# Optimization experiments

Hardware: AMD Instinct MI355X
Metric: run time of the kernel (lower is better)

The kernel has to match this reference:

```python
import jax, jax.numpy as jnp
import numpy as np

B, N, NH, F = 4, 4096, 16, 8      # batch, grid cells, input points per cell, raw features
D, FF, H, PE = 256, 1024, 8, 32   # model_dim, ff_dim, n_heads, pos_emb_dim
NG, NI = 8192, 65536              # grid table size, input-point table size
SEQ = 4                           # 4 ** seq_level
HD = D // H


def layer_norm(x, g, b, eps=1e-5):
    mu = jnp.mean(x, axis=-1, keepdims=True)
    var = jnp.mean(jnp.square(x - mu), axis=-1, keepdims=True)
    return (x - mu) * jax.lax.rsqrt(var + eps) * g + b


def setup_inputs() -> dict:
    key = jax.random.key(0)
    ks = jax.random.split(key, 20)
    inp = {}
    inp["x"] = jax.random.normal(ks[0], (B, N, NH, F), jnp.float32)
    inp["grid_level_indices"] = jax.random.randint(ks[1], (B, N), 0, NG)
    inp["drop_mask"] = jax.random.bernoulli(ks[2], 0.1, (B, N))
    # buffers
    inp["input_mapping"] = jax.random.randint(ks[3], (NG, NH), 0, NI)
    inp["in_range"] = jax.random.bernoulli(ks[4], 0.95, (NG, NH))
    inp["input_coordinates"] = jax.random.uniform(ks[5], (2, NI), jnp.float32, -3.14, 3.14)
    inp["grid_coords"] = jax.random.uniform(ks[6], (2, NG), jnp.float32, -3.14, 3.14)
    # params
    inp["W_in"] = jax.random.normal(ks[7], (F, D), jnp.float32) * 0.05
    inp["b_in"] = jnp.zeros((D,), jnp.float32)
    inp["W_pe"] = jax.random.normal(ks[8], (2, PE), jnp.float32) * 0.2
    inp["W_bias"] = jax.random.normal(ks[9], (PE, H), jnp.float32) * 0.1
    inp["W_v"] = jax.random.normal(ks[10], (D, D), jnp.float32) * 0.02
    inp["W_o"] = jax.random.normal(ks[11], (D, D), jnp.float32) * 0.02
    inp["W1"] = jax.random.normal(ks[12], (D, FF), jnp.float32) * 0.02
    inp["W2"] = jax.random.normal(ks[13], (FF, D), jnp.float32) * 0.02
    inp["g1"] = jnp.ones((D,), jnp.float32)
    inp["b1"] = jnp.zeros((D,), jnp.float32)
    inp["g2"] = jnp.ones((D,), jnp.float32)
    inp["b2"] = jnp.zeros((D,), jnp.float32)
    return inp


def reference(x, grid_level_indices, drop_mask, input_mapping, in_range,
              input_coordinates, grid_coords, W_in, b_in, W_pe, W_bias,
              W_v, W_o, W1, W2, g1, b1, g2, b2):
    b, n, nh, _ = x.shape
    nq = n // SEQ
    K = SEQ * nh  # keys per group

    # input_layer.input_mlp: Linear + SiLU
    x = jax.nn.silu(x @ W_in + b_in)                       # [b,n,nh,D]

    # relative positions (polar): grid-cell coords vs gathered input-point coords
    gseq = grid_level_indices.reshape(b, nq, SEQ)
    idx = input_mapping[gseq]                              # [b,nq,4,nh]
    lon1 = grid_coords[0][gseq][..., None, None]           # [b,nq,4,1,1]
    lat1 = grid_coords[1][gseq][..., None, None]
    lon2 = input_coordinates[0][idx][:, :, None]           # [b,nq,1,4,nh]
    lat2 = input_coordinates[1][idx][:, :, None]
    dlon, dlat = lon2 - lon1, lat2 - lat1                  # [b,nq,4,4,nh]
    dist = jnp.sqrt(dlon * dlon + dlat * dlat + 1e-12)
    ang = jnp.arctan2(dlat, dlon)
    pos1 = dist.reshape(b, nq, SEQ, K)
    pos2 = ang.reshape(b, nq, SEQ, K)

    # mask: out-of-range OR dropped, broadcast across the 4 query cells
    m = (~in_range[grid_level_indices]) | drop_mask[:, :, None]  # [b,n,nh]
    m = m.reshape(b, nq, SEQ, nh)
    mask = jnp.broadcast_to(m[:, :, None], (b, nq, SEQ, SEQ, nh)).reshape(b, nq, SEQ, K)

    xs = x.reshape(b, nq, K, D)                            # kv tokens per group

    # positional bias -> attention scores (qkv_bias=False path: bias-only scores)
    pe = jax.nn.silu(jnp.stack([pos1, pos2], -1) @ W_pe)   # [b,nq,4,K,PE]
    bias = pe @ W_bias                                     # [b,nq,4,K,H]
    scores = jnp.moveaxis(bias, -1, 2)                     # [b,nq,H,4,K]
    scores = jnp.where(mask[:, :, None], -1e9, scores)
    att = jax.nn.softmax(scores, axis=-1)

    vh = (xs @ W_v).reshape(b, nq, K, H, HD)
    out = jnp.einsum('bqhtk,bqkhd->bqthd', att, vh).reshape(b, nq, SEQ, D)
    out = out @ W_o                                        # [b,nq,4,D]

    # nha_layer tail (q_res=False, dropout=0)
    h = layer_norm(out, g1, b1)
    h = layer_norm(h + jax.nn.silu(h @ W1) @ W2, g2, b2)
    return h.reshape(b, n, D)
```

## Files before the change

### kernel.cpp

```cpp
#include <hip/hip_runtime.h>

#define B_   4
#define N_   4096
#define NH_  16
#define F_   8
#define D_   256
#define FF_  1024
#define H_   8
#define PE_  32
#define NG_  8192
#define NI_  65536
#define NQ_  1024

typedef short short8 __attribute__((ext_vector_type(8)));
typedef short short4v __attribute__((ext_vector_type(4)));
typedef float f32x4 __attribute__((ext_vector_type(4)));

__device__ __forceinline__ float silu_f(float v) {
  return v * __builtin_amdgcn_rcpf(1.f + __expf(-v));
}
__device__ __forceinline__ unsigned short f2bf(float f) {
  unsigned int x = __float_as_uint(f);
  unsigned int r = (x + 0x7fffu + ((x >> 16) & 1u)) >> 16;
  return (unsigned short)r;
}
__device__ __forceinline__ float bf2f(unsigned short h) {
  return __uint_as_float(((unsigned int)h) << 16);
}

__device__ __forceinline__ int detect_layout(const unsigned int* w) {
  unsigned b1 = 0, b0 = 0;
#pragma unroll
  for (int i = 0; i < 64; ++i) {
    unsigned v = w[i];
    b1 |= v & 0x0000FF00u;
    b0 |= v & 0x000000FFu;
  }
  return b1 ? 0 : (b0 ? 1 : 2);
}
__device__ __forceinline__ int read_bool(const void* p, int i, int lay) {
  if (lay == 0) return ((const unsigned char*)p)[i] != 0;
  if (lay == 1) return ((const int*)p)[i] != 0;
  return ((const float*)p)[i] != 0.0f;
}

#define WOP_OFF 0
#define W1P_OFF 65536
#define W2P_OFF (65536 + 262144)
#define WVP_OFF (65536 + 262144 + 262144)
#define WIP_OFF (65536 + 262144 + 262144 + 65536)
#define WBP_OFF (WIP_OFF + 8192)
#define WS_TAIL ((65536 + 262144 + 262144) * 2)
#define WS_FULL ((WBP_OFF + 512) * 2)

__global__ __launch_bounds__(256) void k_pack(
    const float* __restrict__ Wo, const float* __restrict__ W1,
    const float* __restrict__ W2, const float* __restrict__ Wv,
    const float* __restrict__ Wi, const float* __restrict__ Wb,
    short* __restrict__ ws)
{
  int t = blockIdx.x * 256 + threadIdx.x;
  if (t < 8192) {
    int g = t & 3, n = (t >> 2) & 255, kk = t >> 10;
    int k0 = kk * 32 + g * 8;
    short8 v;
#pragma unroll
    for (int j = 0; j < 8; ++j) v[j] = (short)f2bf(Wo[(k0 + j) * 256 + n]);
    *(short8*)(ws + WOP_OFF + t * 8) = v;
  } else if (t < 40960) {
    int u = t - 8192;
    int g = u & 3, n = (u >> 2) & 1023, kk = u >> 12;
    int k0 = kk * 32 + g * 8;
    short8 v;
#pragma unroll
    for (int j = 0; j < 8; ++j) v[j] = (short)f2bf(W1[(k0 + j) * 1024 + n]);
    *(short8*)(ws + W1P_OFF + u * 8) = v;
  } else if (t < 73728) {
    int u = t - 40960;
    int g = u & 3, n = (u >> 2) & 255, kk = u >> 10;
    int k0 = kk * 32 + g * 8;
    short8 v;
#pragma unroll
    for (int j = 0; j < 8; ++j) v[j] = (short)f2bf(W2[(k0 + j) * 256 + n]);
    *(short8*)(ws + W2P_OFF + u * 8) = v;
  } else if (t < 81920) {
    int u = t - 73728;
    int g = u & 3, n = (u >> 2) & 255, kk = u >> 10;
    int k0 = kk * 32 + g * 8;
    short8 v;
#pragma unroll
    for (int j = 0; j < 8; ++j) v[j] = (short)f2bf(Wv[(k0 + j) * 256 + n]);
    *(short8*)(ws + WVP_OFF + u * 8) = v;
  } else if (t < 82944) {
    int u = t - 81920;
    int g = u & 3, n = u >> 2;
    short8 v;
#pragma unroll
    for (int j = 0; j < 8; ++j) {
      int k = g * 8 + j;
      v[j] = (k < 8) ? (short)f2bf(Wi[k * 256 + n]) : (short)0;
    }
    *(short8*)(ws + WIP_OFF + (n * 4 + g) * 8) = v;
  } else if (t < 83008) {
    int u = t - 82944;
    int g = u & 3, col = u >> 2;
    short8 v;
#pragma unroll
    for (int j = 0; j < 8; ++j) {
      int p = g * 8 + j;
      v[j] = (col < 8) ? (short)f2bf(Wb[p * 8 + col]) : (short)0;
    }
    *(short8*)(ws + WBP_OFF + (col * 4 + g) * 8) = v;
  }
}

#define OFF_XST   0
#define OFF_ATTB  32768
#define OFF_XL    36864
#define OFF_DIST  36864
#define OFF_ANG   37888
#define OFF_KLON  38912
#define OFF_KLAT  39168
#define OFF_KMSK  39424
#define OFF_GLON  39680
#define OFF_GLAT  39696
#define OFF_GIDX  39712
#define OFF_DROP  39728

__global__ __launch_bounds__(256) void k_attn_mfma(
    const float* __restrict__ x, const int* __restrict__ gli,
    const void* __restrict__ drop, const int* __restrict__ imap,
    const void* __restrict__ inr, const float* __restrict__ icoord,
    const float* __restrict__ gcoord, const float* __restrict__ W_pe,
    const float* __restrict__ b_in, const short* __restrict__ WiP,
    const short* __restrict__ WbP, const short* __restrict__ WvP,
    float* __restrict__ out)
{
  __shared__ __align__(16) char sm[39744];
  float* xl = (float*)(sm + OFF_XL);
  float* distl = (float*)(sm + OFF_DIST);
  float* angl = (float*)(sm + OFF_ANG);
  float* klon = (float*)(sm + OFF_KLON);
  float* klat = (float*)(sm + OFF_KLAT);
  int* kmask = (int*)(sm + OFF_KMSK);
  float* glon = (float*)(sm + OFF_GLON);
  float* glat = (float*)(sm + OFF_GLAT);
  int* gidx = (int*)(sm + OFF_GIDX);
  int* dropf = (int*)(sm + OFF_DROP);

  const int grp = blockIdx.x;
  const int b = grp >> 10;
  const int q = grp & (NQ_ - 1);
  const int tid = threadIdx.x;
  const int w = tid >> 6;
  const int l15 = tid & 15;
  const int g = (tid & 63) >> 4;
  const int swz = (l15 & 7) << 4;

  const int lay = detect_layout((const unsigned int*)inr);

  if (tid < 4) {
    int gg = gli[b * N_ + q * 4 + tid];
    gidx[tid] = gg;
    glon[tid] = gcoord[gg];
    glat[tid] = gcoord[NG_ + gg];
    dropf[tid] = read_bool(drop, b * N_ + q * 4 + tid, lay);
  }
  const float* xb = x + (size_t)(b * N_ + q * 4) * (NH_ * F_);
  xl[tid] = xb[tid];
  xl[tid + 256] = xb[tid + 256];
  __syncthreads();

  if (tid < 64) {
    int s = tid >> 4;
    int gg = gidx[s];
    int id = imap[gg * NH_ + (tid & 15)];
    klon[tid] = icoord[id];
    klat[tid] = icoord[NI_ + id];
    kmask[tid] = (read_bool(inr, gg * NH_ + (tid & 15), lay) == 0) | dropf[s];
  }

  {
    short8 a = {0, 0, 0, 0, 0, 0, 0, 0};
    if (g == 0) {
      const float4* xlf = (const float4*)xl;
      float4 xa = xlf[(w * 16 + l15) * 2];
      float4 xc = xlf[(w * 16 + l15) * 2 + 1];
      a[0] = (short)f2bf(xa.x); a[1] = (short)f2bf(xa.y);
      a[2] = (short)f2bf(xa.z); a[3] = (short)f2bf(xa.w);
      a[4] = (short)f2bf(xc.x); a[5] = (short)f2bf(xc.y);
      a[6] = (short)f2bf(xc.z); a[7] = (short)f2bf(xc.w);
    }
    const int k0 = w * 16 + g * 4;
#pragma unroll
    for (int nf = 0; nf < 16; ++nf) {
      short8 bv = *(const short8*)(WiP + ((nf * 16 + l15) * 4 + g) * 8);
      f32x4 accM = {0.f, 0.f, 0.f, 0.f};
      accM = __builtin_amdgcn_mfma_f32_16x16x32_bf16(a, bv, accM, 0, 0, 0);
      int d = nf * 16 + l15;
      float bn = b_in[d];
      short4v pv;
#pragma unroll
      for (int r = 0; r < 4; ++r)
        pv[r] = (short)f2bf(silu_f(accM[r] + bn));
      *(short4v*)(sm + ((d * 128 + k0 * 2) ^ ((d & 7) << 4))) = pv;
    }
  }
  __syncthreads();

  {
    const int t = tid >> 6, k = tid & 63;
    float dlon = klon[k] - glon[t];
    float dlat = klat[k] - glat[t];
    distl[tid] = sqrtf(dlon * dlon + dlat * dlat + 1e-12f);
    angl[tid] = atan2f(dlat, dlon);
  }
  __syncthreads();

  {
    float wpe0[8], wpe1[8];
    {
      const float4* wp = (const float4*)W_pe;
      float4 w0a = wp[g * 2], w0b = wp[g * 2 + 1];
      float4 w1a = wp[8 + g * 2], w1b = wp[8 + g * 2 + 1];
      wpe0[0] = w0a.x; wpe0[1] = w0a.y; wpe0[2] = w0a.z; wpe0[3] = w0a.w;
      wpe0[4] = w0b.x; wpe0[5] = w0b.y; wpe0[6] = w0b.z; wpe0[7] = w0b.w;
      wpe1[0] = w1a.x; wpe1[1] = w1a.y; wpe1[2] = w1a.z; wpe1[3] = w1a.w;
      wpe1[4] = w1b.x; wpe1[5] = w1b.y; wpe1[6] = w1b.z; wpe1[7] = w1b.w;
    }
    short8 wb = *(const short8*)(WbP + (l15 * 4 + g) * 8);
    f32x4 accS[4];
#pragma unroll
    for (int i = 0; i < 4; ++i) {
      int row = (w * 4 + i) * 16 + l15;
      float dd = distl[row];
      float aa = angl[row];
      short8 pa;
#pragma unroll
      for (int j = 0; j < 8; ++j)
        pa[j] = (short)f2bf(silu_f(fmaf(dd, wpe0[j], aa * wpe1[j])));
      f32x4 z = {0.f, 0.f, 0.f, 0.f};
      accS[i] = __builtin_amdgcn_mfma_f32_16x16x32_bf16(pa, wb, z, 0, 0, 0);
    }
    float sv[16];
    float mx = -1e30f;
#pragma unroll
    for (int i = 0; i < 4; ++i)
#pragma unroll
      for (int r = 0; r < 4; ++r) {
        int k = i * 16 + g * 4 + r;
        float s = kmask[k] ? -1e9f : accS[i][r];
        sv[i * 4 + r] = s;
        mx = fmaxf(mx, s);
      }
    mx = fmaxf(mx, __shfl_xor(mx, 16));
    mx = fmaxf(mx, __shfl_xor(mx, 32));
    float sum = 0.f;
#pragma unroll
    for (int u = 0; u < 16; ++u) { sv[u] = __expf(sv[u] - mx); sum += sv[u]; }
    sum += __shfl_xor(sum, 16);
    sum += __shfl_xor(sum, 32);
    float inv = __builtin_amdgcn_rcpf(sum);
    if (l15 < 8) {
      int row = l15 * 4 + w;
      int rs = (row & 7) << 4;
#pragma unroll
      for (int i = 0; i < 4; ++i) {
        short4v pv;
#pragma unroll
        for (int r = 0; r < 4; ++r) pv[r] = (short)f2bf(sv[i * 4 + r] * inv);
        *(short4v*)(sm + OFF_ATTB + ((row * 128 + (i * 16 + g * 4) * 2) ^ rs)) = pv;
      }
    }
  }
  __syncthreads();

  f32x4 accY[2][4];
  {
    f32x4 z = {0.f, 0.f, 0.f, 0.f};
#pragma unroll
    for (int mi = 0; mi < 2; ++mi)
#pragma unroll
      for (int ni = 0; ni < 4; ++ni) accY[mi][ni] = z;
  }
#pragma unroll
  for (int kk = 0; kk < 2; ++kk) {
    short8 a0 = *(const short8*)(sm + OFF_ATTB + ((l15 * 128 + kk * 64 + g * 16) ^ swz));
    short8 a1 = *(const short8*)(sm + OFF_ATTB + (((16 + l15) * 128 + kk * 64 + g * 16) ^ swz));
    short8 bf[4];
#pragma unroll
    for (int ni = 0; ni < 4; ++ni)
      bf[ni] = *(const short8*)(sm +
          (((w * 64 + ni * 16 + l15) * 128 + kk * 64 + g * 16) ^ swz));
#pragma unroll
    for (int ni = 0; ni < 4; ++ni) {
      accY[0][ni] = __builtin_amdgcn_mfma_f32_16x16x32_bf16(a0, bf[ni], accY[0][ni], 0, 0, 0);
      accY[1][ni] = __builtin_amdgcn_mfma_f32_16x16x32_bf16(a1, bf[ni], accY[1][ni], 0, 0, 0);
    }
  }
  __syncthreads();

#pragma unroll
  for (int mi = 0; mi < 2; ++mi)
#pragma unroll
    for (int ni = 0; ni < 4; ++ni)
#pragma unroll
      for (int r = 0; r < 4; ++r) {
        int row = mi * 16 + g * 4 + r;
        int col = w * 64 + ni * 16 + l15;
        *(unsigned short*)(sm + ((row * 512 + col * 2) ^ ((row & 7) << 4))) =
            f2bf(accY[mi][ni][r]);
      }
  __syncthreads();

  {
    const int mf = w >> 1;
    f32x4 accV[4];
    {
      f32x4 z = {0.f, 0.f, 0.f, 0.f};
#pragma unroll
      for (int ni = 0; ni < 4; ++ni) accV[ni] = z;
    }
#pragma unroll
    for (int kk = 0; kk < 8; ++kk) {
      short8 a = *(const short8*)(sm +
          (((mf * 16 + l15) * 512 + kk * 64 + g * 16) ^ swz));
#pragma unroll
      for (int ni = 0; ni < 4; ++ni) {
        int col = w * 64 + ni * 16 + l15;
        short8 bv = *(const short8*)(WvP + ((size_t)(kk * 256 + col)) * 32 + g * 8);
        accV[ni] = __builtin_amdgcn_mfma_f32_16x16x32_bf16(a, bv, accV[ni], 0, 0, 0);
      }
    }
    float* outl = (float*)(sm + 16384);
    const int gb = (w & 1) * 2;
#pragma unroll
    for (int ni = 0; ni < 4; ++ni) {
      if (g == gb + (ni >> 1)) {
#pragma unroll
        for (int r = 0; r < 4; ++r)
          outl[r * 256 + w * 64 + ni * 16 + l15] = accV[ni][r];
      }
    }
  }
  __syncthreads();

  {
    const float* outl = (const float*)(sm + 16384);
    float* ob = out + (size_t)grp * (4 * D_);
#pragma unroll
    for (int t = 0; t < 4; ++t) ob[t * 256 + tid] = outl[t * 256 + tid];
  }
}

__global__ __launch_bounds__(256) void k_attn_valu(
    const float* __restrict__ x, const int* __restrict__ gli,
    const void* __restrict__ drop, const int* __restrict__ imap,
    const void* __restrict__ inr, const float* __restrict__ icoord,
    const float* __restrict__ gcoord, const float* __restrict__ W_in,
    const float* __restrict__ b_in, const float* __restrict__ W_pe,
    const float* __restrict__ W_bias, const float* __restrict__ W_v,
    float* __restrict__ out)
{
  __shared__ __align__(16) float xl[512];
  __shared__ float glon[4], glat[4];
  __shared__ int gidx[4], dropf[4];
  __shared__ float klon[64], klat[64];
  __shared__ int kmask[64];
  __shared__ __align__(16) unsigned short xs[64 * D_];
  __shared__ __align__(16) float att[32 * 64];
  __shared__ __align__(16) float yl[4 * 8 * 260];

  const int grp = blockIdx.x;
  const int b = grp >> 10;
  const int q = grp & (NQ_ - 1);
  const int tid = threadIdx.x;
  const int lay = detect_layout((const unsigned int*)inr);

  if (tid < 4) {
    int g = gli[b * N_ + q * 4 + tid];
    gidx[tid] = g;
    glon[tid] = gcoord[g];
    glat[tid] = gcoord[NG_ + g];
    dropf[tid] = read_bool(drop, b * N_ + q * 4 + tid, lay);
  }
  const float* xb = x + (size_t)(b * N_ + q * 4) * (NH_ * F_);
  xl[tid] = xb[tid];
  xl[tid + 256] = xb[tid + 256];
  __syncthreads();

  if (tid < 64) {
    int s = tid >> 4;
    int g = gidx[s];
    int id = imap[g * NH_ + (tid & 15)];
    klon[tid] = icoord[id];
    klat[tid] = icoord[NI_ + id];
    kmask[tid] = (read_bool(inr, g * NH_ + (tid & 15), lay) == 0) | dropf[s];
  }
  {
    float w[8];
#pragma unroll
    for (int c = 0; c < 8; ++c) w[c] = W_in[c * D_ + tid];
    float bi = b_in[tid];
#pragma unroll 4
    for (int k = 0; k < 64; ++k) {
      float v = bi;
#pragma unroll
      for (int c = 0; c < 8; ++c) v = fmaf(xl[k * 8 + c], w[c], v);
      xs[k * D_ + tid] = f2bf(silu_f(v));
    }
  }
  __syncthreads();
  {
    const int t = tid >> 6, k = tid & 63;
    float dlon = klon[k] - glon[t];
    float dlat = klat[k] - glat[t];
    float dist = sqrtf(dlon * dlon + dlat * dlat + 1e-12f);
    float ang = atan2f(dlat, dlon);
    float bias[8];
#pragma unroll
    for (int h = 0; h < 8; ++h) bias[h] = 0.f;
#pragma unroll
    for (int p = 0; p < 32; ++p) {
      float pv = silu_f(fmaf(dist, W_pe[p], ang * W_pe[32 + p]));
#pragma unroll
      for (int h = 0; h < 8; ++h) bias[h] = fmaf(pv, W_bias[p * 8 + h], bias[h]);
    }
    const bool mk = (kmask[k] != 0);
#pragma unroll
    for (int h = 0; h < 8; ++h)
      att[(h * 4 + t) * 64 + k] = mk ? -1e9f : bias[h];
  }
  __syncthreads();
  {
    const int row = tid >> 3, l8 = tid & 7;
    float sv[8];
    float mx = -1e30f;
#pragma unroll
    for (int i = 0; i < 8; ++i) { sv[i] = att[row * 64 + l8 + i * 8]; mx = fmaxf(mx, sv[i]); }
#pragma unroll
    for (int off = 1; off < 8; off <<= 1) mx = fmaxf(mx, __shfl_xor(mx, off, 8));
    float sm = 0.f;
#pragma unroll
    for (int i = 0; i < 8; ++i) { sv[i] = __expf(sv[i] - mx); sm += sv[i]; }
#pragma unroll
    for (int off = 1; off < 8; off <<= 1) sm += __shfl_xor(sm, off, 8);
    float inv = 1.f / sm;
#pragma unroll
    for (int i = 0; i < 8; ++i) att[row * 64 + l8 + i * 8] = sv[i] * inv;
  }
  __syncthreads();
  {
    float acc[32];
#pragma unroll
    for (int r = 0; r < 32; ++r) acc[r] = 0.f;
    for (int k4 = 0; k4 < 64; k4 += 4) {
      float xv0 = bf2f(xs[(k4 + 0) * D_ + tid]);
      float xv1 = bf2f(xs[(k4 + 1) * D_ + tid]);
      float xv2 = bf2f(xs[(k4 + 2) * D_ + tid]);
      float xv3 = bf2f(xs[(k4 + 3) * D_ + tid]);
#pragma unroll
      for (int r = 0; r < 32; ++r) {
        float4 a = *(const float4*)&att[r * 64 + k4];
        acc[r] = fmaf(a.x, xv0, acc[r]);
        acc[r] = fmaf(a.y, xv1, acc[r]);
        acc[r] = fmaf(a.z, xv2, acc[r]);
        acc[r] = fmaf(a.w, xv3, acc[r]);
      }
    }
#pragma unroll
    for (int r = 0; r < 32; ++r)
      yl[(r & 3) * 2080 + (r >> 2) * 260 + tid] = acc[r];
  }
  __syncthreads();
  {
    const int h = tid >> 5;
    float o0 = 0.f, o1 = 0.f, o2 = 0.f, o3 = 0.f;
    for (int c = 0; c < 256; c += 4) {
      float w0 = W_v[(c + 0) * D_ + tid];
      float w1 = W_v[(c + 1) * D_ + tid];
      float w2 = W_v[(c + 2) * D_ + tid];
      float w3 = W_v[(c + 3) * D_ + tid];
      float4 y0 = *(const float4*)&yl[0 * 2080 + h * 260 + c];
      float4 y1 = *(const float4*)&yl[1 * 2080 + h * 260 + c];
      float4 y2 = *(const float4*)&yl[2 * 2080 + h * 260 + c];
      float4 y3 = *(const float4*)&yl[3 * 2080 + h * 260 + c];
      o0 = fmaf(y0.x, w0, o0); o0 = fmaf(y0.y, w1, o0); o0 = fmaf(y0.z, w2, o0); o0 = fmaf(y0.w, w3, o0);
      o1 = fmaf(y1.x, w0, o1); o1 = fmaf(y1.y, w1, o1); o1 = fmaf(y1.z, w2, o1); o1 = fmaf(y1.w, w3, o1);
      o2 = fmaf(y2.x, w0, o2); o2 = fmaf(y2.y, w1, o2); o2 = fmaf(y2.z, w2, o2); o2 = fmaf(y2.w, w3, o2);
      o3 = fmaf(y3.x, w0, o3); o3 = fmaf(y3.y, w1, o3); o3 = fmaf(y3.z, w2, o3); o3 = fmaf(y3.w, w3, o3);
    }
    float* ob = out + (size_t)grp * (4 * D_);
    ob[0 * D_ + tid] = o0;
    ob[1 * D_ + tid] = o1;
    ob[2 * D_ + tid] = o2;
    ob[3 * D_ + tid] = o3;
  }
}

__device__ __forceinline__ void gemm_acc8(
    f32x4 acc[4][4], const unsigned short* As, const short* Bp,
    int N, int kk0, int colbase, int l15, int g)
{
#pragma unroll
  for (int kk = 0; kk < 8; ++kk) {
    short8 a[4], bv[4];
#pragma unroll
    for (int mi = 0; mi < 4; ++mi) {
      int row = mi * 16 + l15;
      int byte = (row * 512 + kk * 64 + g * 16) ^ ((row & 7) << 4);
      a[mi] = *(const short8*)((const char*)As + byte);
    }
#pragma unroll
    for (int ni = 0; ni < 4; ++ni) {
      int col = colbase + ni * 16 + l15;
      size_t off = ((size_t)(kk0 + kk) * N + col) * 32 + g * 8;
      bv[ni] = *(const short8*)(Bp + off);
    }
#pragma unroll
    for (int mi = 0; mi < 4; ++mi)
#pragma unroll
      for (int ni = 0; ni < 4; ++ni)
        acc[mi][ni] = __builtin_amdgcn_mfma_f32_16x16x32_bf16(
            a[mi], bv[ni], acc[mi][ni], 0, 0, 0);
  }
}

__global__ __launch_bounds__(256) void k_tail_mfma(
    const float* __restrict__ g1v, const float* __restrict__ b1v,
    const float* __restrict__ g2v, const float* __restrict__ b2v,
    const short* __restrict__ WoP, const short* __restrict__ W1P,
    const short* __restrict__ W2P, float* __restrict__ io)
{
  __shared__ __align__(16) unsigned short sA1[64 * 256];
  __shared__ __align__(16) unsigned short sU[64 * 256];
  __shared__ float sPs[4][64];
  __shared__ float sPss[4][64];

  const int tid = threadIdx.x;
  const int w = tid >> 6;
  const int l = tid & 63;
  const int l15 = l & 15;
  const int g = l >> 4;
  float* base = io + (size_t)blockIdx.x * (64 * 256);

#pragma unroll
  for (int i = 0; i < 16; ++i) {
    int e = (tid + 256 * i) * 4;
    int row = e >> 8, c = e & 255;
    float4 v = *(const float4*)(base + e);
    unsigned int lo = (unsigned int)f2bf(v.x) | ((unsigned int)f2bf(v.y) << 16);
    unsigned int hi = (unsigned int)f2bf(v.z) | ((unsigned int)f2bf(v.w) << 16);
    int byte = (row * 512 + c * 2) ^ ((row & 7) << 4);
    *(uint2*)((char*)sU + byte) = make_uint2(lo, hi);
  }
  __syncthreads();

  f32x4 acc[4][4];
  {
    f32x4 z = {0.f, 0.f, 0.f, 0.f};
#pragma unroll
    for (int mi = 0; mi < 4; ++mi)
#pragma unroll
      for (int ni = 0; ni < 4; ++ni) acc[mi][ni] = z;
  }
  gemm_acc8(acc, sU, WoP, 256, 0, w * 64, l15, g);

#pragma unroll
  for (int mi = 0; mi < 4; ++mi)
#pragma unroll
    for (int r = 0; r < 4; ++r) {
      float a0 = acc[mi][0][r], a1 = acc[mi][1][r], a2 = acc[mi][2][r], a3 = acc[mi][3][r];
      float s = a0 + a1 + a2 + a3;
      float ss = a0 * a0 + a1 * a1 + a2 * a2 + a3 * a3;
#pragma unroll
      for (int off = 1; off < 16; off <<= 1) {
        s += __shfl_xor(s, off);
        ss += __shfl_xor(ss, off);
      }
      if (l15 == 0) {
        int row = 16 * mi + 4 * g + r;
        sPs[w][row] = s;
        sPss[w][row] = ss;
      }
    }
  __syncthreads();

  {
    float ga[4], bb[4];
#pragma unroll
    for (int ni = 0; ni < 4; ++ni) {
      int col = 64 * w + 16 * ni + l15;
      ga[ni] = g1v[col];
      bb[ni] = b1v[col];
    }
#pragma unroll
    for (int mi = 0; mi < 4; ++mi)
#pragma unroll
      for (int r = 0; r < 4; ++r) {
        int row = 16 * mi + 4 * g + r;
        float S = sPs[0][row] + sPs[1][row] + sPs[2][row] + sPs[3][row];
        float SS = sPss[0][row] + sPss[1][row] + sPss[2][row] + sPss[3][row];
        float mu = S * (1.f / 256.f);
        float rs = rsqrtf(SS * (1.f / 256.f) - mu * mu + 1e-5f);
#pragma unroll
        for (int ni = 0; ni < 4; ++ni) {
          int col = 64 * w + 16 * ni + l15;
          float val = (acc[mi][ni][r] - mu) * rs * ga[ni] + bb[ni];
          acc[mi][ni][r] = val;
          int byte = (row * 512 + col * 2) ^ ((row & 7) << 4);
          *(unsigned short*)((char*)sA1 + byte) = f2bf(val);
        }
      }
  }
  __syncthreads();

  for (int p = 0; p < 4; ++p) {
    f32x4 acc2[4][4];
    {
      f32x4 z = {0.f, 0.f, 0.f, 0.f};
#pragma unroll
      for (int mi = 0; mi < 4; ++mi)
#pragma unroll
        for (int ni = 0; ni < 4; ++ni) acc2[mi][ni] = z;
    }
    gemm_acc8(acc2, sA1, W1P, 1024, 0, p * 256 + w * 64, l15, g);
#pragma unroll
    for (int mi = 0; mi < 4; ++mi)
#pragma unroll
      for (int ni = 0; ni < 4; ++ni)
#pragma unroll
        for (int r = 0; r < 4; ++r) {
          int row = 16 * mi + 4 * g + r;
          int col = 64 * w + 16 * ni + l15;
          int byte = (row * 512 + col * 2) ^ ((row & 7) << 4);
          *(unsigned short*)((char*)sU + byte) = f2bf(silu_f(acc2[mi][ni][r]));
        }
    __syncthreads();
    gemm_acc8(acc, sU, W2P, 256, p * 8, w * 64, l15, g);
    __syncthreads();
  }

#pragma unroll
  for (int mi = 0; mi < 4; ++mi)
#pragma unroll
    for (int r = 0; r < 4; ++r) {
      float a0 = acc[mi][0][r], a1 = acc[mi][1][r], a2 = acc[mi][2][r], a3 = acc[mi][3][r];
      float s = a0 + a1 + a2 + a3;
      float ss = a0 * a0 + a1 * a1 + a2 * a2 + a3 * a3;
#pragma unroll
      for (int off = 1; off < 16; off <<= 1) {
        s += __shfl_xor(s, off);
        ss += __shfl_xor(ss, off);
      }
      if (l15 == 0) {
        int row = 16 * mi + 4 * g + r;
        sPs[w][row] = s;
        sPss[w][row] = ss;
      }
    }
  __syncthreads();

  {
    float ga[4], bb[4];
#pragma unroll
    for (int ni = 0; ni < 4; ++ni) {
      int col = 64 * w + 16 * ni + l15;
      ga[ni] = g2v[col];
      bb[ni] = b2v[col];
    }
#pragma unroll
    for (int mi = 0; mi < 4; ++mi)
#pragma unroll
      for (int r = 0; r < 4; ++r) {
        int row = 16 * mi + 4 * g + r;
        float S = sPs[0][row] + sPs[1][row] + sPs[2][row] + sPs[3][row];
        float SS = sPss[0][row] + sPss[1][row] + sPss[2][row] + sPss[3][row];
        float mu = S * (1.f / 256.f);
        float rs = rsqrtf(SS * (1.f / 256.f) - mu * mu + 1e-5f);
#pragma unroll
        for (int ni = 0; ni < 4; ++ni) {
          int col = 64 * w + 16 * ni + l15;
          base[row * 256 + col] = (acc[mi][ni][r] - mu) * rs * ga[ni] + bb[ni];
        }
      }
  }
}

__global__ __launch_bounds__(256) void k_tail(
    const float* __restrict__ Wo, const float* __restrict__ W1,
    const float* __restrict__ W2, const float* __restrict__ g1,
    const float* __restrict__ b1, const float* __restrict__ g2,
    const float* __restrict__ b2, float* __restrict__ io)
{
  __shared__ __align__(16) float rl[16 * 260];
  __shared__ __align__(16) float h1[16 * 260];
  __shared__ __align__(16) unsigned short u[16 * FF_];
  const int tid = threadIdx.x;
  float* base = io + (size_t)blockIdx.x * (16 * D_);

#pragma unroll
  for (int r = 0; r < 16; ++r) rl[r * 260 + tid] = base[r * D_ + tid];
  __syncthreads();
  {
    float acc[16];
#pragma unroll
    for (int r = 0; r < 16; ++r) acc[r] = 0.f;
    for (int c = 0; c < 256; c += 4) {
      float w0 = Wo[(c + 0) * D_ + tid], w1 = Wo[(c + 1) * D_ + tid];
      float w2 = Wo[(c + 2) * D_ + tid], w3 = Wo[(c + 3) * D_ + tid];
#pragma unroll
      for (int r = 0; r < 16; ++r) {
        float4 rv = *(const float4*)&rl[r * 260 + c];
        acc[r] = fmaf(rv.x, w0, acc[r]); acc[r] = fmaf(rv.y, w1, acc[r]);
        acc[r] = fmaf(rv.z, w2, acc[r]); acc[r] = fmaf(rv.w, w3, acc[r]);
      }
    }
#pragma unroll
    for (int r = 0; r < 16; ++r) h1[r * 260 + tid] = acc[r];
  }
  __syncthreads();
  {
    const int r = tid >> 4, l = tid & 15;
    float s = 0.f, ss = 0.f;
#pragma unroll
    for (int i = 0; i < 16; ++i) { float v = h1[r * 260 + l + i * 16]; s += v; ss += v * v; }
#pragma unroll
    for (int off = 1; off < 16; off <<= 1) { s += __shfl_xor(s, off, 16); ss += __shfl_xor(ss, off, 16); }
    float mu = s * (1.f / 256.f);
    float rs = rsqrtf(ss * (1.f / 256.f) - mu * mu + 1e-5f);
#pragma unroll
    for (int i = 0; i < 16; ++i) {
      int d = l + i * 16;
      h1[r * 260 + d] = (h1[r * 260 + d] - mu) * rs * g1[d] + b1[d];
    }
  }
  __syncthreads();
  for (int fo = 0; fo < 4; ++fo) {
    const int f = fo * 256 + tid;
    float a2[16];
#pragma unroll
    for (int r = 0; r < 16; ++r) a2[r] = 0.f;
    for (int c = 0; c < 256; c += 4) {
      float w0 = W1[(c + 0) * FF_ + f], w1 = W1[(c + 1) * FF_ + f];
      float w2 = W1[(c + 2) * FF_ + f], w3 = W1[(c + 3) * FF_ + f];
#pragma unroll
      for (int r = 0; r < 16; ++r) {
        float4 hv = *(const float4*)&h1[r * 260 + c];
        a2[r] = fmaf(hv.x, w0, a2[r]); a2[r] = fmaf(hv.y, w1, a2[r]);
        a2[r] = fmaf(hv.z, w2, a2[r]); a2[r] = fmaf(hv.w, w3, a2[r]);
      }
    }
#pragma unroll
    for (int r = 0; r < 16; ++r) u[r * FF_ + f] = f2bf(silu_f(a2[r]));
  }
  __syncthreads();
  {
    float a3[16];
#pragma unroll
    for (int r = 0; r < 16; ++r) a3[r] = h1[r * 260 + tid];
    for (int f = 0; f < FF_; f += 8) {
      float w[8];
#pragma unroll
      for (int i = 0; i < 8; ++i) w[i] = W2[(f + i) * D_ + tid];
#pragma unroll
      for (int r = 0; r < 16; ++r) {
        uint4 uv = *(const uint4*)&u[r * FF_ + f];
        a3[r] = fmaf(__uint_as_float(uv.x << 16), w[0], a3[r]);
        a3[r] = fmaf(__uint_as_float(uv.x & 0xffff0000u), w[1], a3[r]);
        a3[r] = fmaf(__uint_as_float(uv.y << 16), w[2], a3[r]);
        a3[r] = fmaf(__uint_as_float(uv.y & 0xffff0000u), w[3], a3[r]);
        a3[r] = fmaf(__uint_as_float(uv.z << 16), w[4], a3[r]);
        a3[r] = fmaf(__uint_as_float(uv.z & 0xffff0000u), w[5], a3[r]);
        a3[r] = fmaf(__uint_as_float(uv.w << 16), w[6], a3[r]);
        a3[r] = fmaf(__uint_as_float(uv.w & 0xffff0000u), w[7], a3[r]);
      }
    }
#pragma unroll
    for (int r = 0; r < 16; ++r) rl[r * 260 + tid] = a3[r];
  }
  __syncthreads();
  {
    const int r = tid >> 4, l = tid & 15;
    float s = 0.f, ss = 0.f;
#pragma unroll
    for (int i = 0; i < 16; ++i) { float v = rl[r * 260 + l + i * 16]; s += v; ss += v * v; }
#pragma unroll
    for (int off = 1; off < 16; off <<= 1) { s += __shfl_xor(s, off, 16); ss += __shfl_xor(ss, off, 16); }
    float mu = s * (1.f / 256.f);
    float rs = rsqrtf(ss * (1.f / 256.f) - mu * mu + 1e-5f);
#pragma unroll
    for (int i = 0; i < 16; ++i) {
      int d = l + i * 16;
      base[r * D_ + d] = (rl[r * 260 + d] - mu) * rs * g2[d] + b2[d];
    }
  }
}

extern "C" void kernel_launch(void* const* d_in, const int* in_sizes, int n_in,
                              void* d_out, int out_size, void* d_ws, size_t ws_size,
                              hipStream_t stream) {
  (void)in_sizes; (void)n_in; (void)out_size;
  const float* x = (const float*)d_in[0];
  const int* gli = (const int*)d_in[1];
  const void* drop = d_in[2];
  const int* imap = (const int*)d_in[3];
  const void* inr = d_in[4];
  const float* icoord = (const float*)d_in[5];
  const float* gcoord = (const float*)d_in[6];
  const float* W_in = (const float*)d_in[7];
  const float* b_in = (const float*)d_in[8];
  const float* W_pe = (const float*)d_in[9];
  const float* W_bias = (const float*)d_in[10];
  const float* W_v = (const float*)d_in[11];
  const float* W_o = (const float*)d_in[12];
  const float* W1 = (const float*)d_in[13];
  const float* W2 = (const float*)d_in[14];
  const float* g1 = (const float*)d_in[15];
  const float* b1 = (const float*)d_in[16];
  const float* g2 = (const float*)d_in[17];
  const float* b2 = (const float*)d_in[18];
  float* out = (float*)d_out;

  if (ws_size >= (size_t)WS_FULL) {
    short* ws = (short*)d_ws;
    k_pack<<<dim3(325), dim3(256), 0, stream>>>(W_o, W1, W2, W_v, W_in, W_bias, ws);
    k_attn_mfma<<<dim3(B_ * NQ_), dim3(256), 0, stream>>>(
        x, gli, drop, imap, inr, icoord, gcoord, W_pe, b_in,
        ws + WIP_OFF, ws + WBP_OFF, ws + WVP_OFF, out);
    k_tail_mfma<<<dim3((B_ * N_) / 64), dim3(256), 0, stream>>>(
        g1, b1, g2, b2, ws + WOP_OFF, ws + W1P_OFF, ws + W2P_OFF, out);
  } else if (ws_size >= (size_t)WS_TAIL) {
    short* ws = (short*)d_ws;
    k_pack<<<dim3(325), dim3(256), 0, stream>>>(W_o, W1, W2, W_v, W_in, W_bias, ws);
    k_attn_valu<<<dim3(B_ * NQ_), dim3(256), 0, stream>>>(
        x, gli, drop, imap, inr, icoord, gcoord, W_in, b_in, W_pe, W_bias, W_v, out);
    k_tail_mfma<<<dim3((B_ * N_) / 64), dim3(256), 0, stream>>>(
        g1, b1, g2, b2, ws + WOP_OFF, ws + W1P_OFF, ws + W2P_OFF, out);
  } else {
    k_attn_valu<<<dim3(B_ * NQ_), dim3(256), 0, stream>>>(
        x, gli, drop, imap, inr, icoord, gcoord, W_in, b_in, W_pe, W_bias, W_v, out);
    k_tail<<<dim3((B_ * N_) / 16), dim3(256), 0, stream>>>(
        W_o, W1, W2, g1, b1, g2, b2, out);
  }
}
```

Before: 132.7 us.

## Use hardware packed bf16 conversion and halve tail MFMA tile rows to 32

Replaces the software round-to-nearest float-to-bf16 routine with the v_cvt_pk_bf16_f32 instruction, converting two values per instruction in the attention and tail kernels. The tail MFMA kernel now processes 32 rows per block instead of 64, halving shared memory and accumulator registers and doubling the grid. This aims to cut VALU conversion overhead and raise occupancy and parallelism in the tail kernel, at the cost of reloading the packed weight tiles twice as often across blocks.

```diff
diff --git a/kernel.cpp b/kernel.cpp
--- a/kernel.cpp
+++ b/kernel.cpp
@@ -16,6 +16,8 @@
 typedef short short4v __attribute__((ext_vector_type(4)));
 typedef float f32x4 __attribute__((ext_vector_type(4)));
 
+union U8 { short8 s8; uint4 u4; };
+
 __device__ __forceinline__ float silu_f(float v) {
   return v * __builtin_amdgcn_rcpf(1.f + __expf(-v));
 }
@@ -23,6 +25,14 @@
   unsigned int x = __float_as_uint(f);
   unsigned int r = (x + 0x7fffu + ((x >> 16) & 1u)) >> 16;
   return (unsigned short)r;
+}
+__device__ __forceinline__ unsigned int cvt_pk(float a, float b) {
+  unsigned int r;
+  asm("v_cvt_pk_bf16_f32 %0, %1, %2" : "=v"(r) : "v"(a), "v"(b));
+  return r;
+}
+__device__ __forceinline__ unsigned short f2bf1(float v) {
+  return (unsigned short)cvt_pk(v, v);
 }
 __device__ __forceinline__ float bf2f(unsigned short h) {
   return __uint_as_float(((unsigned int)h) << 16);
@@ -186,10 +196,12 @@
       const float4* xlf = (const float4*)xl;
       float4 xa = xlf[(w * 16 + l15) * 2];
       float4 xc = xlf[(w * 16 + l15) * 2 + 1];
-      a[0] = (short)f2bf(xa.x); a[1] = (short)f2bf(xa.y);
-      a[2] = (short)f2bf(xa.z); a[3] = (short)f2bf(xa.w);
-      a[4] = (short)f2bf(xc.x); a[5] = (short)f2bf(xc.y);
-      a[6] = (short)f2bf(xc.z); a[7] = (short)f2bf(xc.w);
+      U8 u;
+      u.u4.x = cvt_pk(xa.x, xa.y);
+      u.u4.y = cvt_pk(xa.z, xa.w);
+      u.u4.z = cvt_pk(xc.x, xc.y);
+      u.u4.w = cvt_pk(xc.z, xc.w);
+      a = u.s8;
     }
     const int k0 = w * 16 + g * 4;
 #pragma unroll
@@ -199,11 +211,10 @@
       accM = __builtin_amdgcn_mfma_f32_16x16x32_bf16(a, bv, accM, 0, 0, 0);
       int d = nf * 16 + l15;
       float bn = b_in[d];
-      short4v pv;
-#pragma unroll
-      for (int r = 0; r < 4; ++r)
-        pv[r] = (short)f2bf(silu_f(accM[r] + bn));
-      *(short4v*)(sm + ((d * 128 + k0 * 2) ^ ((d & 7) << 4))) = pv;
+      uint2 pv;
+      pv.x = cvt_pk(silu_f(accM[0] + bn), silu_f(accM[1] + bn));
+      pv.y = cvt_pk(silu_f(accM[2] + bn), silu_f(accM[3] + bn));
+      *(uint2*)(sm + ((d * 128 + k0 * 2) ^ ((d & 7) << 4))) = pv;
     }
   }
   __syncthreads();
@@ -235,12 +246,17 @@
       int row = (w * 4 + i) * 16 + l15;
       float dd = distl[row];
       float aa = angl[row];
-      short8 pa;
+      float pe[8];
 #pragma unroll
       for (int j = 0; j < 8; ++j)
-        pa[j] = (short)f2bf(silu_f(fmaf(dd, wpe0[j], aa * wpe1[j])));
+        pe[j] = silu_f(fmaf(dd, wpe0[j], aa * wpe1[j]));
+      U8 pu;
+      pu.u4.x = cvt_pk(pe[0], pe[1]);
+      pu.u4.y = cvt_pk(pe[2], pe[3]);
+      pu.u4.z = cvt_pk(pe[4], pe[5]);
+      pu.u4.w = cvt_pk(pe[6], pe[7]);
       f32x4 z = {0.f, 0.f, 0.f, 0.f};
-      accS[i] = __builtin_amdgcn_mfma_f32_16x16x32_bf16(pa, wb, z, 0, 0, 0);
+      accS[i] = __builtin_amdgcn_mfma_f32_16x16x32_bf16(pu.s8, wb, z, 0, 0, 0);
     }
     float sv[16];
     float mx = -1e30f;
@@ -266,10 +282,10 @@
       int rs = (row & 7) << 4;
 #pragma unroll
       for (int i = 0; i < 4; ++i) {
-        short4v pv;
-#pragma unroll
-        for (int r = 0; r < 4; ++r) pv[r] = (short)f2bf(sv[i * 4 + r] * inv);
-        *(short4v*)(sm + OFF_ATTB + ((row * 128 + (i * 16 + g * 4) * 2) ^ rs)) = pv;
+        uint2 pv;
+        pv.x = cvt_pk(sv[i * 4 + 0] * inv, sv[i * 4 + 1] * inv);
+        pv.y = cvt_pk(sv[i * 4 + 2] * inv, sv[i * 4 + 3] * inv);
+        *(uint2*)(sm + OFF_ATTB + ((row * 128 + (i * 16 + g * 4) * 2) ^ rs)) = pv;
       }
     }
   }
@@ -309,7 +325,7 @@
         int row = mi * 16 + g * 4 + r;
         int col = w * 64 + ni * 16 + l15;
         *(unsigned short*)(sm + ((row * 512 + col * 2) ^ ((row & 7) << 4))) =
-            f2bf(accY[mi][ni][r]);
+            f2bf1(accY[mi][ni][r]);
       }
   __syncthreads();
 
@@ -498,18 +514,19 @@
   }
 }
 
-__device__ __forceinline__ void gemm_acc8(
-    f32x4 acc[4][4], const unsigned short* As, const short* Bp,
+template<int MI>
+__device__ __forceinline__ void gemm_mfma(
+    f32x4 acc[MI][4], const char* As, const short* Bp,
     int N, int kk0, int colbase, int l15, int g)
 {
 #pragma unroll
   for (int kk = 0; kk < 8; ++kk) {
-    short8 a[4], bv[4];
-#pragma unroll
-    for (int mi = 0; mi < 4; ++mi) {
+    short8 a[MI], bv[4];
+#pragma unroll
+    for (int mi = 0; mi < MI; ++mi) {
       int row = mi * 16 + l15;
       int byte = (row * 512 + kk * 64 + g * 16) ^ ((row & 7) << 4);
-      a[mi] = *(const short8*)((const char*)As + byte);
+      a[mi] = *(const short8*)(As + byte);
     }
 #pragma unroll
     for (int ni = 0; ni < 4; ++ni) {
@@ -518,7 +535,7 @@
       bv[ni] = *(const short8*)(Bp + off);
     }
 #pragma unroll
-    for (int mi = 0; mi < 4; ++mi)
+    for (int mi = 0; mi < MI; ++mi)
 #pragma unroll
       for (int ni = 0; ni < 4; ++ni)
         acc[mi][ni] = __builtin_amdgcn_mfma_f32_16x16x32_bf16(
@@ -532,42 +549,42 @@
     const short* __restrict__ WoP, const short* __restrict__ W1P,
     const short* __restrict__ W2P, float* __restrict__ io)
 {
-  __shared__ __align__(16) unsigned short sA1[64 * 256];
-  __shared__ __align__(16) unsigned short sU[64 * 256];
-  __shared__ float sPs[4][64];
-  __shared__ float sPss[4][64];
+  __shared__ __align__(16) unsigned short sA1[32 * 256];
+  __shared__ __align__(16) unsigned short sU[32 * 256];
+  __shared__ float sPs[4][32];
+  __shared__ float sPss[4][32];
 
   const int tid = threadIdx.x;
   const int w = tid >> 6;
-  const int l = tid & 63;
-  const int l15 = l & 15;
-  const int g = l >> 4;
-  float* base = io + (size_t)blockIdx.x * (64 * 256);
-
-#pragma unroll
-  for (int i = 0; i < 16; ++i) {
+  const int l15 = tid & 15;
+  const int g = (tid & 63) >> 4;
+  float* base = io + (size_t)blockIdx.x * (32 * 256);
+
+#pragma unroll
+  for (int i = 0; i < 8; ++i) {
     int e = (tid + 256 * i) * 4;
     int row = e >> 8, c = e & 255;
     float4 v = *(const float4*)(base + e);
-    unsigned int lo = (unsigned int)f2bf(v.x) | ((unsigned int)f2bf(v.y) << 16);
-    unsigned int hi = (unsigned int)f2bf(v.z) | ((unsigned int)f2bf(v.w) << 16);
+    uint2 pv;
+    pv.x = cvt_pk(v.x, v.y);
+    pv.y = cvt_pk(v.z, v.w);
     int byte = (row * 512 + c * 2) ^ ((row & 7) << 4);
-    *(uint2*)((char*)sU + byte) = make_uint2(lo, hi);
-  }
-  __syncthreads();
-
-  f32x4 acc[4][4];
+    *(uint2*)((char*)sU + byte) = pv;
+  }
+  __syncthreads();
+
+  f32x4 acc[2][4];
   {
     f32x4 z = {0.f, 0.f, 0.f, 0.f};
 #pragma unroll
-    for (int mi = 0; mi < 4; ++mi)
+    for (int mi = 0; mi < 2; ++mi)
 #pragma unroll
       for (int ni = 0; ni < 4; ++ni) acc[mi][ni] = z;
   }
-  gemm_acc8(acc, sU, WoP, 256, 0, w * 64, l15, g);
-
-#pragma unroll
-  for (int mi = 0; mi < 4; ++mi)
+  gemm_mfma<2>(acc, (const char*)sU, WoP, 256, 0, w * 64, l15, g);
+
+#pragma unroll
+  for (int mi = 0; mi < 2; ++mi)
 #pragma unroll
     for (int r = 0; r < 4; ++r) {
       float a0 = acc[mi][0][r], a1 = acc[mi][1][r], a2 = acc[mi][2][r], a3 = acc[mi][3][r];
@@ -595,7 +612,7 @@
       bb[ni] = b1v[col];
     }
 #pragma unroll
-    for (int mi = 0; mi < 4; ++mi)
+    for (int mi = 0; mi < 2; ++mi)
 #pragma unroll
       for (int r = 0; r < 4; ++r) {
         int row = 16 * mi + 4 * g + r;
@@ -609,24 +626,24 @@
           float val = (acc[mi][ni][r] - mu) * rs * ga[ni] + bb[ni];
           acc[mi][ni][r] = val;
           int byte = (row * 512 + col * 2) ^ ((row & 7) << 4);
-          *(unsigned short*)((char*)sA1 + byte) = f2bf(val);
+          *(unsigned short*)((char*)sA1 + byte) = f2bf1(val);
         }
       }
   }
   __syncthreads();
 
   for (int p = 0; p < 4; ++p) {
-    f32x4 acc2[4][4];
+    f32x4 acc2[2][4];
     {
       f32x4 z = {0.f, 0.f, 0.f, 0.f};
 #pragma unroll
-      for (int mi = 0; mi < 4; ++mi)
+      for (int mi = 0; mi < 2; ++mi)
 #pragma unroll
         for (int ni = 0; ni < 4; ++ni) acc2[mi][ni] = z;
     }
-    gemm_acc8(acc2, sA1, W1P, 1024, 0, p * 256 + w * 64, l15, g);
-#pragma unroll
-    for (int mi = 0; mi < 4; ++mi)
+    gemm_mfma<2>(acc2, (const char*)sA1, W1P, 1024, 0, p * 256 + w * 64, l15, g);
+#pragma unroll
+    for (int mi = 0; mi < 2; ++mi)
 #pragma unroll
       for (int ni = 0; ni < 4; ++ni)
 #pragma unroll
@@ -634,15 +651,15 @@
           int row = 16 * mi + 4 * g + r;
           int col = 64 * w + 16 * ni + l15;
           int byte = (row * 512 + col * 2) ^ ((row & 7) << 4);
-          *(unsigned short*)((char*)sU + byte) = f2bf(silu_f(acc2[mi][ni][r]));
+          *(unsigned short*)((char*)sU + byte) = f2bf1(silu_f(acc2[mi][ni][r]));
         }
     __syncthreads();
-    gemm_acc8(acc, sU, W2P, 256, p * 8, w * 64, l15, g);
+    gemm_mfma<2>(acc, (const char*)sU, W2P, 256, p * 8, w * 64, l15, g);
     __syncthreads();
   }
 
 #pragma unroll
-  for (int mi = 0; mi < 4; ++mi)
+  for (int mi = 0; mi < 2; ++mi)
 #pragma unroll
     for (int r = 0; r < 4; ++r) {
       float a0 = acc[mi][0][r], a1 = acc[mi][1][r], a2 = acc[mi][2][r], a3 = acc[mi][3][r];
@@ -670,7 +687,7 @@
       bb[ni] = b2v[col];
     }
 #pragma unroll
-    for (int mi = 0; mi < 4; ++mi)
+    for (int mi = 0; mi < 2; ++mi)
 #pragma unroll
       for (int r = 0; r < 4; ++r) {
         int row = 16 * mi + 4 * g + r;
@@ -828,14 +845,14 @@
     k_attn_mfma<<<dim3(B_ * NQ_), dim3(256), 0, stream>>>(
         x, gli, drop, imap, inr, icoord, gcoord, W_pe, b_in,
         ws + WIP_OFF, ws + WBP_OFF, ws + WVP_OFF, out);
-    k_tail_mfma<<<dim3((B_ * N_) / 64), dim3(256), 0, stream>>>(
+    k_tail_mfma<<<dim3((B_ * N_) / 32), dim3(256), 0, stream>>>(
         g1, b1, g2, b2, ws + WOP_OFF, ws + W1P_OFF, ws + W2P_OFF, out);
   } else if (ws_size >= (size_t)WS_TAIL) {
     short* ws = (short*)d_ws;
     k_pack<<<dim3(325), dim3(256), 0, stream>>>(W_o, W1, W2, W_v, W_in, W_bias, ws);
     k_attn_valu<<<dim3(B_ * NQ_), dim3(256), 0, stream>>>(
         x, gli, drop, imap, inr, icoord, gcoord, W_in, b_in, W_pe, W_bias, W_v, out);
-    k_tail_mfma<<<dim3((B_ * N_) / 64), dim3(256), 0, stream>>>(
+    k_tail_mfma<<<dim3((B_ * N_) / 32), dim3(256), 0, stream>>>(
         g1, b1, g2, b2, ws + WOP_OFF, ws + W1P_OFF, ws + W2P_OFF, out);
   } else {
     k_attn_valu<<<dim3(B_ * NQ_), dim3(256), 0, stream>>>(
```

After: 115.7 us. 12.8% less time.
